# Kernel optimization log

Hardware: AMD Instinct MI355X
Metric: run time of the kernel (lower is better)

The kernel has to match this reference:

```python
import jax, jax.numpy as jnp
import numpy as np

NUM_DENSE = 13
NUM_SPARSE = 26
FEAT_NUM = 40000  # categories per sparse field
FEATURE_LENGTH = NUM_SPARSE * FEAT_NUM + NUM_DENSE  # 1_040_013
K = 64
BATCH = 4096


def setup_inputs() -> dict:
    key = jax.random.key(0)
    k1, k2, k3, k4 = jax.random.split(key, 4)
    dense_inputs = jax.random.normal(k1, (BATCH, NUM_DENSE), dtype=jnp.float32)
    sparse_inputs = jax.random.randint(k2, (BATCH, NUM_SPARSE), 0, FEAT_NUM, dtype=jnp.int64)
    w0 = jnp.zeros((1,), dtype=jnp.float32)
    w = jax.random.normal(k3, (FEATURE_LENGTH, 1), dtype=jnp.float32) * 0.05
    V = jax.random.normal(k4, (K, FEATURE_LENGTH), dtype=jnp.float32) * 0.05
    return {"dense_inputs": dense_inputs, "sparse_inputs": sparse_inputs, "w0": w0, "w": w, "V": V}


def reference(dense_inputs, sparse_inputs, w0, w, V):
    # Feature layout matches the original concat order: [dense (NUM_DENSE) | one-hot field 0 | ... | one-hot field 25].
    # The one-hot @ matrix products are computed as row gathers (mathematically identical,
    # since one_hot(i) @ M == M[i]).
    offsets = NUM_DENSE + FEAT_NUM * jnp.arange(NUM_SPARSE, dtype=sparse_inputs.dtype)
    idx = sparse_inputs + offsets[None, :]  # [B, NUM_SPARSE] global row ids into feature_length

    # ---- first order: w0 + stack @ w ----
    w_dense = w[:NUM_DENSE]            # [ND, 1]
    first = w0 + dense_inputs @ w_dense + jnp.sum(w[idx, 0], axis=1, keepdims=True)  # [B,1]

    # ---- second order: 0.5 * sum((stack @ V^T)^2 - (stack^2 @ (V^T)^2), axis=1) ----
    Vt = V.T                           # [F, K]
    Vt_dense = Vt[:NUM_DENSE]          # [ND, K]
    Vt_sparse = Vt[idx]                # [B, NUM_SPARSE, K] gathered latent vectors

    sv = dense_inputs @ Vt_dense + jnp.sum(Vt_sparse, axis=1)                 # [B, K]
    # stack^2 for the one-hot block equals the one-hot block itself (0/1 entries)
    s2v2 = (dense_inputs ** 2) @ (Vt_dense ** 2) + jnp.sum(Vt_sparse ** 2, axis=1)  # [B, K]

    second = 0.5 * jnp.sum(sv ** 2 - s2v2, axis=1, keepdims=True)  # [B,1]
    return first + second
```

## Files before the change

### kernel.cpp

```cpp
#include <hip/hip_runtime.h>

#define NUM_DENSE 13
#define NUM_SPARSE 26
#define FEAT_NUM 40000
#define FEATURE_LENGTH (NUM_SPARSE * FEAT_NUM + NUM_DENSE)
#define KDIM 64
#define BATCH 4096
#define QSIZE 10000
#define NT 1024

__global__ void transpose_kernel(const int* __restrict__ sp, int* __restrict__ sp_t) {
    int tid = blockIdx.x * blockDim.x + threadIdx.x;
    int j = tid >> 12;
    int b = tid & 4095;
    sp_t[tid] = sp[b * NUM_SPARSE + j];
}

__global__ __launch_bounds__(NT) void accum_kernel(const float* __restrict__ V,
                                                   const int* __restrict__ sp_t,
                                                   float* __restrict__ PS,
                                                   float* __restrict__ PQ) {
    __shared__ __align__(16) float win[QSIZE + 4];

    const int k = blockIdx.x;
    const int g = blockIdx.y;
    const int jstart = g * 7 - (g > 2 ? (g - 2) : 0);
    const int jend   = jstart + (g < 2 ? 7 : 6);
    const int tid = threadIdx.x;

    float sAcc[4] = {0.f, 0.f, 0.f, 0.f};
    float qAcc[4] = {0.f, 0.f, 0.f, 0.f};

    for (int j = jstart; j < jend; ++j) {
        int spv[4];
#pragma unroll
        for (int r = 0; r < 4; ++r) spv[r] = sp_t[j * BATCH + tid + NT * r];

        for (int q = 0; q < 4; ++q) {
            const size_t s0 = (size_t)k * FEATURE_LENGTH + NUM_DENSE
                            + (size_t)j * FEAT_NUM + q * QSIZE;
            const float* __restrict__ Vq = V + s0;
            const int h   = (4 - ((int)(s0 & 3))) & 3;
            const int off = (4 - h) & 3;
            const int n4  = (QSIZE - h) >> 2;
            const int tl  = (QSIZE - h) & 3;

            __syncthreads();
            if (tid < h) win[off + tid] = Vq[tid];
            const float4* __restrict__ Vq4 = (const float4*)(Vq + h);
            for (int m = tid; m < n4; m += NT) {
                float4 v = Vq4[m];
                *reinterpret_cast<float4*>(&win[off + h + 4 * m]) = v;
            }
            const int ts = h + 4 * n4;
            if (tid < tl) win[off + ts + tid] = Vq[ts + tid];
            __syncthreads();

            const int q0 = q * QSIZE;
#pragma unroll
            for (int r = 0; r < 4; ++r) {
                int rel = spv[r] - q0;
                bool in = (rel >= 0) && (rel < QSIZE);
                int a = in ? (rel + off) : 0;
                float v = win[a];
                v = in ? v : 0.f;
                sAcc[r] += v;
                qAcc[r] += v * v;
            }
        }
    }

    const int base = (g * KDIM + k) * BATCH + tid;
#pragma unroll
    for (int r = 0; r < 4; ++r) {
        PS[base + NT * r] = sAcc[r];
        PQ[base + NT * r] = qAcc[r];
    }
}

__global__ void final_kernel(const float* __restrict__ dense,
                             const float* __restrict__ w0,
                             const float* __restrict__ w,
                             const float* __restrict__ V,
                             const int* __restrict__ sp_t,
                             const float* __restrict__ PS,
                             const float* __restrict__ PQ,
                             float* __restrict__ out) {
    const int wave = threadIdx.x >> 6;
    const int lane = threadIdx.x & 63;
    const int b = blockIdx.x * 4 + wave;
    const int k = lane;
    const float* __restrict__ Vk = V + (size_t)k * FEATURE_LENGTH;

    float sv = 0.f, qv = 0.f;
#pragma unroll
    for (int g = 0; g < 4; ++g) {
        sv += PS[(g * KDIM + k) * BATCH + b];
        qv += PQ[(g * KDIM + k) * BATCH + b];
    }
#pragma unroll
    for (int d = 0; d < NUM_DENSE; ++d) {
        float x  = dense[b * NUM_DENSE + d];
        float vv = Vk[d];
        sv += x * vv;
        qv += x * x * vv * vv;
    }
    float t = 0.5f * (sv * sv - qv);

    if (lane < NUM_SPARSE)
        t += w[NUM_DENSE + lane * FEAT_NUM + sp_t[lane * BATCH + b]];
    if (lane >= 32 && lane < 32 + NUM_DENSE) {
        int d = lane - 32;
        t += dense[b * NUM_DENSE + d] * w[d];
    }

#pragma unroll
    for (int off = 32; off > 0; off >>= 1) t += __shfl_down(t, off);
    if (lane == 0) out[b] = w0[0] + t;
}

extern "C" void kernel_launch(void* const* d_in, const int* in_sizes, int n_in,
                              void* d_out, int out_size, void* d_ws, size_t ws_size,
                              hipStream_t stream) {
    const float* dense  = (const float*)d_in[0];
    const int*   sparse = (const int*)d_in[1];
    const float* w0     = (const float*)d_in[2];
    const float* w      = (const float*)d_in[3];
    const float* V      = (const float*)d_in[4];
    float* out = (float*)d_out;

    char* ws = (char*)d_ws;
    int*   sp_t = (int*)ws;
    float* PS   = (float*)(ws + (1 << 19));
    float* PQ   = (float*)(ws + (1 << 19) + 4 * KDIM * BATCH * 4);

    transpose_kernel<<<(NUM_SPARSE * BATCH) / 256, 256, 0, stream>>>(sparse, sp_t);
    accum_kernel<<<dim3(KDIM, 4), NT, 0, stream>>>(V, sp_t, PS, PQ);
    final_kernel<<<BATCH / 4, 256, 0, stream>>>(dense, w0, w, V, sp_t, PS, PQ, out);
}
```

Measured before the change: 406.9 us.

## Double-buffer V chunk loads in LDS and remap final kernel to batch-per-lane

The accumulation kernel now streams V in 8000-float chunks into two LDS buffers. The next chunk's global loads are issued before the current chunk's lookups, so each step needs only one barrier and load latency overlaps with compute. Alignment handling is simplified by loading from an aligned base offset. The final kernel maps batch rows to lanes and splits K across waves, giving coalesced PS/PQ reads and an LDS reduction instead of a shuffle reduction. The field split across groups is also rebalanced. The cost is more LDS use and more register pressure in both kernels.

```diff
diff --git a/kernel.cpp b/kernel.cpp
--- a/kernel.cpp
+++ b/kernel.cpp
@@ -6,7 +6,9 @@
 #define FEATURE_LENGTH (NUM_SPARSE * FEAT_NUM + NUM_DENSE)
 #define KDIM 64
 #define BATCH 4096
-#define QSIZE 10000
+#define QSIZE 8000
+#define NCHUNK 5
+#define LDSN (QSIZE + 4)
 #define NT 1024
 
 __global__ void transpose_kernel(const int* __restrict__ sp, int* __restrict__ sp_t) {
@@ -20,54 +22,82 @@
                                                    const int* __restrict__ sp_t,
                                                    float* __restrict__ PS,
                                                    float* __restrict__ PQ) {
-    __shared__ __align__(16) float win[QSIZE + 4];
+    __shared__ __align__(16) float buf[2][LDSN];
 
     const int k = blockIdx.x;
     const int g = blockIdx.y;
-    const int jstart = g * 7 - (g > 2 ? (g - 2) : 0);
-    const int jend   = jstart + (g < 2 ? 7 : 6);
+    const int jstart = (g * NUM_SPARSE) / 4;
+    const int jend   = ((g + 1) * NUM_SPARSE) / 4;
     const int tid = threadIdx.x;
+
+    const size_t kbase = (size_t)k * FEATURE_LENGTH + NUM_DENSE;
+    const int a   = (int)(kbase & 3);
+    const int nl4 = (QSIZE + a + 3) >> 2;
+
+    const int nstage = (jend - jstart) * NCHUNK;
 
     float sAcc[4] = {0.f, 0.f, 0.f, 0.f};
     float qAcc[4] = {0.f, 0.f, 0.f, 0.f};
 
-    for (int j = jstart; j < jend; ++j) {
-        int spv[4];
+    int j = jstart, q = 0;
+    int spv[4];
 #pragma unroll
-        for (int r = 0; r < 4; ++r) spv[r] = sp_t[j * BATCH + tid + NT * r];
+    for (int r = 0; r < 4; ++r) spv[r] = sp_t[j * BATCH + tid + NT * r];
 
-        for (int q = 0; q < 4; ++q) {
-            const size_t s0 = (size_t)k * FEATURE_LENGTH + NUM_DENSE
-                            + (size_t)j * FEAT_NUM + q * QSIZE;
-            const float* __restrict__ Vq = V + s0;
-            const int h   = (4 - ((int)(s0 & 3))) & 3;
-            const int off = (4 - h) & 3;
-            const int n4  = (QSIZE - h) >> 2;
-            const int tl  = (QSIZE - h) & 3;
+    {
+        const float4* __restrict__ g4 =
+            (const float4*)(V + (kbase + (size_t)j * FEAT_NUM) - a);
+        float4 v0 = g4[tid];
+        bool p1 = (tid + NT) < nl4;
+        float4 v1;
+        if (p1) v1 = g4[tid + NT];
+        *reinterpret_cast<float4*>(&buf[0][4 * tid]) = v0;
+        if (p1) *reinterpret_cast<float4*>(&buf[0][4 * (tid + NT)]) = v1;
+    }
+    __syncthreads();
 
-            __syncthreads();
-            if (tid < h) win[off + tid] = Vq[tid];
-            const float4* __restrict__ Vq4 = (const float4*)(Vq + h);
-            for (int m = tid; m < n4; m += NT) {
-                float4 v = Vq4[m];
-                *reinterpret_cast<float4*>(&win[off + h + 4 * m]) = v;
-            }
-            const int ts = h + 4 * n4;
-            if (tid < tl) win[off + ts + tid] = Vq[ts + tid];
-            __syncthreads();
+    int cur = 0;
+    for (int s = 0; s < nstage; ++s) {
+        int qn = q + 1, jn = j;
+        if (qn == NCHUNK) { qn = 0; jn = j + 1; }
+        const bool hasNext = (s + 1 < nstage);
 
+        float4 v0, v1;
+        bool p1 = false;
+        if (hasNext) {
+            const float4* __restrict__ g4 =
+                (const float4*)(V + (kbase + (size_t)jn * FEAT_NUM + (size_t)qn * QSIZE) - a);
+            v0 = g4[tid];
+            p1 = (tid + NT) < nl4;
+            if (p1) v1 = g4[tid + NT];
+        }
+
+        {
             const int q0 = q * QSIZE;
 #pragma unroll
             for (int r = 0; r < 4; ++r) {
                 int rel = spv[r] - q0;
                 bool in = (rel >= 0) && (rel < QSIZE);
-                int a = in ? (rel + off) : 0;
-                float v = win[a];
+                int addr = in ? (rel + a) : 0;
+                float v = buf[cur][addr];
                 v = in ? v : 0.f;
                 sAcc[r] += v;
                 qAcc[r] += v * v;
             }
         }
+
+        if (hasNext) {
+            *reinterpret_cast<float4*>(&buf[cur ^ 1][4 * tid]) = v0;
+            if (p1) *reinterpret_cast<float4*>(&buf[cur ^ 1][4 * (tid + NT)]) = v1;
+        }
+        __syncthreads();
+        cur ^= 1;
+
+        if (hasNext && jn != j) {
+#pragma unroll
+            for (int r = 0; r < 4; ++r) spv[r] = sp_t[jn * BATCH + tid + NT * r];
+        }
+        j = jn; q = qn;
     }
 
     const int base = (g * KDIM + k) * BATCH + tid;
@@ -78,45 +108,59 @@
     }
 }
 
-__global__ void final_kernel(const float* __restrict__ dense,
-                             const float* __restrict__ w0,
-                             const float* __restrict__ w,
-                             const float* __restrict__ V,
-                             const int* __restrict__ sp_t,
-                             const float* __restrict__ PS,
-                             const float* __restrict__ PQ,
-                             float* __restrict__ out) {
-    const int wave = threadIdx.x >> 6;
-    const int lane = threadIdx.x & 63;
-    const int b = blockIdx.x * 4 + wave;
-    const int k = lane;
-    const float* __restrict__ Vk = V + (size_t)k * FEATURE_LENGTH;
+__global__ __launch_bounds__(256) void final_kernel(const float* __restrict__ dense,
+                                                    const float* __restrict__ w0,
+                                                    const float* __restrict__ w,
+                                                    const float* __restrict__ V,
+                                                    const int* __restrict__ sp_t,
+                                                    const float* __restrict__ PS,
+                                                    const float* __restrict__ PQ,
+                                                    float* __restrict__ out) {
+    __shared__ float red[4][64];
+    const int wv = threadIdx.x >> 6;
+    const int ln = threadIdx.x & 63;
+    const int b  = blockIdx.x * 64 + ln;
 
-    float sv = 0.f, qv = 0.f;
-#pragma unroll
-    for (int g = 0; g < 4; ++g) {
-        sv += PS[(g * KDIM + k) * BATCH + b];
-        qv += PQ[(g * KDIM + k) * BATCH + b];
-    }
+    float x[NUM_DENSE], x2[NUM_DENSE];
 #pragma unroll
     for (int d = 0; d < NUM_DENSE; ++d) {
-        float x  = dense[b * NUM_DENSE + d];
-        float vv = Vk[d];
-        sv += x * vv;
-        qv += x * x * vv * vv;
-    }
-    float t = 0.5f * (sv * sv - qv);
-
-    if (lane < NUM_SPARSE)
-        t += w[NUM_DENSE + lane * FEAT_NUM + sp_t[lane * BATCH + b]];
-    if (lane >= 32 && lane < 32 + NUM_DENSE) {
-        int d = lane - 32;
-        t += dense[b * NUM_DENSE + d] * w[d];
+        x[d]  = dense[b * NUM_DENSE + d];
+        x2[d] = x[d] * x[d];
     }
 
+    float t = 0.f;
+    const int k0 = wv * 16;
+#pragma unroll 4
+    for (int kk = 0; kk < 16; ++kk) {
+        const int k = k0 + kk;
+        float sv = 0.f, qv = 0.f;
 #pragma unroll
-    for (int off = 32; off > 0; off >>= 1) t += __shfl_down(t, off);
-    if (lane == 0) out[b] = w0[0] + t;
+        for (int g = 0; g < 4; ++g) {
+            sv += PS[((g << 6) + k) * BATCH + b];
+            qv += PQ[((g << 6) + k) * BATCH + b];
+        }
+        const float* __restrict__ Vk = V + (size_t)k * FEATURE_LENGTH;
+#pragma unroll
+        for (int d = 0; d < NUM_DENSE; ++d) {
+            float vv = Vk[d];
+            sv += x[d] * vv;
+            qv += x2[d] * vv * vv;
+        }
+        t += sv * sv - qv;
+    }
+    t *= 0.5f;
+
+    for (int jj = wv; jj < NUM_SPARSE; jj += 4)
+        t += w[NUM_DENSE + jj * FEAT_NUM + sp_t[jj * BATCH + b]];
+    if (wv == 0) {
+#pragma unroll
+        for (int d = 0; d < NUM_DENSE; ++d) t += x[d] * w[d];
+    }
+
+    red[wv][ln] = t;
+    __syncthreads();
+    if (wv == 0)
+        out[b] = w0[0] + red[0][ln] + red[1][ln] + red[2][ln] + red[3][ln];
 }
 
 extern "C" void kernel_launch(void* const* d_in, const int* in_sizes, int n_in,
@@ -136,5 +180,5 @@
 
     transpose_kernel<<<(NUM_SPARSE * BATCH) / 256, 256, 0, stream>>>(sparse, sp_t);
     accum_kernel<<<dim3(KDIM, 4), NT, 0, stream>>>(V, sp_t, PS, PQ);
-    final_kernel<<<BATCH / 4, 256, 0, stream>>>(dense, w0, w, V, sp_t, PS, PQ, out);
+    final_kernel<<<BATCH / 64, 256, 0, stream>>>(dense, w0, w, V, sp_t, PS, PQ, out);
 }
```

Measured after the change: 401.2 us. Within noise of the previous version (-1.4%).
